# Kernel optimization log

Measured on AMD Instinct MI355X. Metric: run time of the kernel, lower is better.

## Reference

```python
import jax, jax.numpy as jnp
import numpy as np

# Architecture constants (match init_kwargs)
STEPS, BATCH = 256, 128
IN_SIZE, H1, H2, OUT = 512, 1536, 1536, 512
DELAY = 1


def setup_inputs() -> dict:
    key = jax.random.key(0)
    ks = jax.random.split(key, 5)
    def init_w(k, shape):
        fan_in = shape[0]
        return (jax.random.normal(k, shape, jnp.float32) / np.sqrt(fan_in).astype(np.float32))
    return {
        "inputs": jax.random.normal(ks[0], (STEPS, BATCH, IN_SIZE), jnp.float32),
        # hidden1 RNNC: in = sizes['#input'] + sizes['hidden1'] (self-recurrent conn)
        "W1": init_w(ks[1], (IN_SIZE + H1, H1)),
        "b1": jnp.zeros((H1,), jnp.float32),
        # hidden2 RNNC: in = sizes['hidden1'] + sizes['hidden2']
        "W2": init_w(ks[2], (H1 + H2, H2)),
        "b2": jnp.zeros((H2,), jnp.float32),
        # '##output' PlaceholderWt: linear readout from hidden2
        "Wo": init_w(ks[3], (H2, OUT)),
        "bo": jnp.zeros((OUT,), jnp.float32),
    }


def reference(inputs, W1, b1, W2, b2, Wo, bo):
    # Stepped multi-layer RNN with delay=1 spike buffers.
    # Within a step, layers update in order, so a layer reading spikes_all[-1]
    # of an EARLIER layer sees the current step's spike, while self/backward
    # connections see the previous step's spike (carried through the scan).
    B = inputs.shape[1]

    def step(carry, x_t):
        s_h1_prev, s_h2_prev = carry
        s_in = x_t                                               # Placeholder '#input'
        # hidden1: prevs = ['#input' (current), 'hidden1' (prev step)]
        s_h1 = jnp.tanh(jnp.concatenate([s_in, s_h1_prev], -1) @ W1 + b1)
        # hidden2: prevs = ['hidden1' (current), 'hidden2' (prev step)]
        s_h2 = jnp.tanh(jnp.concatenate([s_h1, s_h2_prev], -1) @ W2 + b2)
        # '##output' PlaceholderWt: linear readout of current hidden2 spike
        out = s_h2 @ Wo + bo
        return (s_h1, s_h2), out

    init = (jnp.zeros((B, H1), inputs.dtype), jnp.zeros((B, H2), inputs.dtype))
    _, outs = jax.lax.scan(step, init, inputs)                   # [steps, B, OUT]
    # spikes_all includes `delay` initial zero spikes from reset_state
    zeros = jnp.zeros((DELAY, B, OUT), inputs.dtype)
    return jnp.concatenate([zeros, outs], axis=0)                # [delay+steps, B, OUT]
```

## Files before the change

kernel.cpp:

```cpp
#include <hip/hip_runtime.h>
#include <math.h>

#define STEPS 256
#define BATCH 128
#define HALF_M 64
#define INSZ  512
#define H1SZ  1536
#define H2SZ  1536
#define NOUT  512
#define K1    2048
#define K2    3072
#define NC1   48
#define NC2   48
#define NC3   16
#define NBLK  224

typedef short bf16x8 __attribute__((ext_vector_type(8)));
typedef float f32x4  __attribute__((ext_vector_type(4)));
typedef unsigned short u16;

__device__ __forceinline__ f32x4 mfma16(bf16x8 a, bf16x8 b, f32x4 c) {
  return __builtin_amdgcn_mfma_f32_16x16x32_bf16(a, b, c, 0, 0, 0);
}

__device__ __forceinline__ u16 f2bf(float f) {
  unsigned u = __builtin_bit_cast(unsigned, f);
  u += 0x7fffu + ((u >> 16) & 1u);
  return (u16)(u >> 16);
}

__device__ __forceinline__ bf16x8 cvt8(const float* p) {
  f32x4 lo = *(const f32x4*)p;
  f32x4 hi = *(const f32x4*)(p + 4);
  union { unsigned u[4]; bf16x8 v; } r;
  asm("v_cvt_pk_bf16_f32 %0, %1, %2" : "=v"(r.u[0]) : "v"(lo[0]), "v"(lo[1]));
  asm("v_cvt_pk_bf16_f32 %0, %1, %2" : "=v"(r.u[1]) : "v"(lo[2]), "v"(lo[3]));
  asm("v_cvt_pk_bf16_f32 %0, %1, %2" : "=v"(r.u[2]) : "v"(hi[0]), "v"(hi[1]));
  asm("v_cvt_pk_bf16_f32 %0, %1, %2" : "=v"(r.u[3]) : "v"(hi[2]), "v"(hi[3]));
  return r.v;
}

#define LOAD_SC_OFS(dst, ptr, ofs) \
  asm volatile("global_load_dwordx4 %0, %1, off offset:%2 sc0 sc1" \
               : "=v"(dst) : "v"(ptr), "i"(ofs) : "memory")
#define STORE_SC(ptr, val) \
  asm volatile("global_store_dwordx4 %0, %1, off sc0 sc1" :: "v"(ptr), "v"(val) : "memory")
#define WAITV(n) asm volatile("s_waitcnt vmcnt(" #n ")" ::: "memory")
#define PIN4(v) asm volatile("" : "+v"(v))

__device__ __forceinline__ void set_flag(int* p, int v) {
  __hip_atomic_store(p, v, __ATOMIC_RELAXED, __HIP_MEMORY_SCOPE_SYSTEM);
}

__device__ __forceinline__ void wave_wait(const int* p, int tgt, bool active) {
  while (true) {
    int v = __hip_atomic_load(p, __ATOMIC_RELAXED, __HIP_MEMORY_SCOPE_SYSTEM);
    if (!__any(active && (v < tgt))) break;
    __builtin_amdgcn_s_sleep(1);
  }
}

__device__ __forceinline__ void kloop12(const u16* base, const bf16x8 (*Br)[2],
                                        f32x4 (*acc)[2], int r16) {
  const u16* rp[4];
#pragma unroll
  for (int mf = 0; mf < 4; ++mf) rp[mf] = base + (size_t)(mf * 16 + r16) * 1536;
  bf16x8 A[8][4];
  WAITV(0);
#pragma unroll
  for (int d = 0; d < 8; ++d)
#pragma unroll
    for (int mf = 0; mf < 4; ++mf)
      LOAD_SC_OFS(A[d][mf], rp[mf], d * 64);
#pragma unroll
  for (int ks = 0; ks < 12; ++ks) {
    const int rem = (11 - ks) < 7 ? (11 - ks) : 7;
    if (rem == 7)      WAITV(28);
    else if (rem == 6) WAITV(24);
    else if (rem == 5) WAITV(20);
    else if (rem == 4) WAITV(16);
    else if (rem == 3) WAITV(12);
    else if (rem == 2) WAITV(8);
    else if (rem == 1) WAITV(4);
    else               WAITV(0);
    __builtin_amdgcn_sched_barrier(0);
#pragma unroll
    for (int mf = 0; mf < 4; ++mf) {
      acc[mf][0] = mfma16(A[ks & 7][mf], Br[ks][0], acc[mf][0]);
      acc[mf][1] = mfma16(A[ks & 7][mf], Br[ks][1], acc[mf][1]);
    }
    if (ks < 4) {
#pragma unroll
      for (int mf = 0; mf < 4; ++mf)
        LOAD_SC_OFS(A[ks & 7][mf], rp[mf], (ks + 8) * 64);
    }
  }
}

__device__ __forceinline__ void kloop_x4(const float* xb, const bf16x8 (*Br)[2],
                                         f32x4 (*acc)[2], int r16) {
#pragma unroll
  for (int ks = 0; ks < 4; ++ks)
#pragma unroll
    for (int mf = 0; mf < 4; ++mf) {
      bf16x8 a = cvt8(xb + (size_t)(mf * 16 + r16) * INSZ + ks * 32);
      acc[mf][0] = mfma16(a, Br[ks][0], acc[mf][0]);
      acc[mf][1] = mfma16(a, Br[ks][1], acc[mf][1]);
    }
}

__device__ __forceinline__ void store_red(float (*red)[64][36], int kw, int kg, int r16,
                                          const f32x4 (*acc)[2]) {
#pragma unroll
  for (int mf = 0; mf < 4; ++mf)
#pragma unroll
    for (int nf = 0; nf < 2; ++nf)
#pragma unroll
      for (int r = 0; r < 4; ++r)
        red[kw][mf * 16 + kg * 4 + r][nf * 16 + r16] = acc[mf][nf][r];
}

__device__ __forceinline__ void epi_tanh(const float (*red)[64][36], f32x4 bv0, f32x4 bv1,
                                         u16* dstbase, int n0, int tid) {
  const int row = tid >> 2, c0 = (tid & 3) * 8;
  f32x4 s0 = bv0, s1 = bv1;
#pragma unroll
  for (int w = 0; w < 4; ++w) {
    s0 += *(const f32x4*)&red[w][row][c0];
    s1 += *(const f32x4*)&red[w][row][c0 + 4];
  }
  float t[8];
#pragma unroll
  for (int j = 0; j < 4; ++j) t[j] = tanhf(s0[j]);
#pragma unroll
  for (int j = 0; j < 4; ++j) t[4 + j] = tanhf(s1[j]);
  union { unsigned u[4]; bf16x8 v; } pk;
  asm("v_cvt_pk_bf16_f32 %0, %1, %2" : "=v"(pk.u[0]) : "v"(t[0]), "v"(t[1]));
  asm("v_cvt_pk_bf16_f32 %0, %1, %2" : "=v"(pk.u[1]) : "v"(t[2]), "v"(t[3]));
  asm("v_cvt_pk_bf16_f32 %0, %1, %2" : "=v"(pk.u[2]) : "v"(t[4]), "v"(t[5]));
  asm("v_cvt_pk_bf16_f32 %0, %1, %2" : "=v"(pk.u[3]) : "v"(t[6]), "v"(t[7]));
  u16* dst = dstbase + (size_t)row * 1536 + n0 + c0;
  STORE_SC(dst, pk.v);
}

__global__ __launch_bounds__(256)
__attribute__((amdgpu_waves_per_eu(1, 1)))
void rnn_main(
    const float* __restrict__ x,
    const u16* __restrict__ W1T, const u16* __restrict__ W2T, const u16* __restrict__ WoT,
    const float* __restrict__ b1, const float* __restrict__ b2, const float* __restrict__ bo,
    u16* __restrict__ h1ring, u16* __restrict__ h2ring,
    float* __restrict__ out, int* __restrict__ bar)
{
  __shared__ float red[4][64][36];
  const int tid = threadIdx.x;
  const int kw = tid >> 6, lane = tid & 63;
  const int r16 = lane & 15, kg = lane >> 4;
  const int bid = blockIdx.x;

  int grp, half, col;
  if (bid < 2 * NC1)              { grp = 0; half = bid / NC1;         col = bid % NC1; }
  else if (bid < 2 * (NC1 + NC2)) { grp = 1; half = (bid - 96) / NC2;  col = (bid - 96) % NC2; }
  else                            { grp = 2; half = (bid - 192) / NC3; col = (bid - 192) % NC3; }
  const int n0 = col * 32;
  int* f1 = bar + (half * NC1) * 16;
  int* f2 = bar + (96 + half * NC2) * 16;
  int* f3 = bar + (192 + half * NC3) * 16;

  u16* h1base = h1ring + (size_t)half * 4 * HALF_M * H1SZ;
  u16* h2base = h2ring + (size_t)half * 4 * HALF_M * H2SZ;

  const int* wpA = f1; int dA = 0; bool aA = false;
  const int* wpB = f1; int dB = 0; bool aB = false;
  if (grp == 0) {
    if (lane < 12)                      { wpA = f1 + (kw * 12 + lane) * 16; dA = 0;  aA = true; }
    else if (kw == 0 && lane >= 16)     { wpA = f2 + (lane - 16) * 16;      dA = -3; aA = true; }
  } else if (grp == 1) {
    if (lane < 12) {
      wpA = f2 + (kw * 12 + lane) * 16; dA = 0; aA = true;
      wpB = f1 + (kw * 12 + lane) * 16; dB = 1; aB = true;
    } else if (kw == 0 && lane >= 32 && lane < 48) {
      wpA = f3 + (lane - 32) * 16; dA = -3; aA = true;
    }
  } else {
    if (lane < 12)                      { wpA = f2 + (kw * 12 + lane) * 16; dA = 1;  aA = true; }
  }

  if (grp == 0) {
    bf16x8 BrX[4][2], Brh[12][2];
#pragma unroll
    for (int ks = 0; ks < 4; ++ks)
#pragma unroll
      for (int nf = 0; nf < 2; ++nf)
        BrX[ks][nf] = *(const bf16x8*)(W1T + (size_t)(n0 + nf * 16 + r16) * K1
                                       + kw * 128 + ks * 32 + kg * 8);
#pragma unroll
    for (int ks = 0; ks < 12; ++ks)
#pragma unroll
      for (int nf = 0; nf < 2; ++nf)
        Brh[ks][nf] = *(const bf16x8*)(W1T + (size_t)(n0 + nf * 16 + r16) * K1
                                       + 512 + kw * 384 + ks * 32 + kg * 8);
#pragma unroll
    for (int ks = 0; ks < 4; ++ks) { PIN4(BrX[ks][0]); PIN4(BrX[ks][1]); }
#pragma unroll
    for (int ks = 0; ks < 12; ++ks) { PIN4(Brh[ks][0]); PIN4(Brh[ks][1]); }
    const f32x4 bv0 = *(const f32x4*)(b1 + n0 + (tid & 3) * 8);
    const f32x4 bv1 = *(const f32x4*)(b1 + n0 + (tid & 3) * 8 + 4);

    for (int k = 0; k < STEPS; ++k) {
      f32x4 acc[4][2] = {};
      const float* xb = x + ((size_t)k * BATCH + half * HALF_M) * INSZ + kw * 128 + kg * 8;
      kloop_x4(xb, BrX, acc, r16);
      wave_wait(wpA, k + dA, aA);
      kloop12(h1base + (size_t)((k + 3) & 3) * HALF_M * H1SZ + kw * 384 + kg * 8,
              Brh, acc, r16);
      store_red(red, kw, kg, r16, acc);
      __syncthreads();
      epi_tanh(red, bv0, bv1, h1base + (size_t)(k & 3) * HALF_M * H1SZ, n0, tid);
      WAITV(0);
      __syncthreads();
      if (tid == 0) set_flag(&f1[col * 16], k + 1);
    }
  } else if (grp == 1) {
    bf16x8 Bh2[12][2], Bh1[12][2];
#pragma unroll
    for (int ks = 0; ks < 12; ++ks)
#pragma unroll
      for (int nf = 0; nf < 2; ++nf) {
        Bh2[ks][nf] = *(const bf16x8*)(W2T + (size_t)(n0 + nf * 16 + r16) * K2
                                       + 1536 + kw * 384 + ks * 32 + kg * 8);
        Bh1[ks][nf] = *(const bf16x8*)(W2T + (size_t)(n0 + nf * 16 + r16) * K2
                                       + kw * 384 + ks * 32 + kg * 8);
      }
#pragma unroll
    for (int ks = 0; ks < 12; ++ks) { PIN4(Bh2[ks][0]); PIN4(Bh2[ks][1]);
                                      PIN4(Bh1[ks][0]); PIN4(Bh1[ks][1]); }
    const f32x4 bv0 = *(const f32x4*)(b2 + n0 + (tid & 3) * 8);
    const f32x4 bv1 = *(const f32x4*)(b2 + n0 + (tid & 3) * 8 + 4);

    for (int j = 0; j < STEPS; ++j) {
      f32x4 acc[4][2] = {};
      wave_wait(wpA, j + dA, aA);
      kloop12(h2base + (size_t)((j + 3) & 3) * HALF_M * H2SZ + kw * 384 + kg * 8,
              Bh2, acc, r16);
      wave_wait(wpB, j + dB, aB);
      kloop12(h1base + (size_t)(j & 3) * HALF_M * H1SZ + kw * 384 + kg * 8,
              Bh1, acc, r16);
      store_red(red, kw, kg, r16, acc);
      __syncthreads();
      epi_tanh(red, bv0, bv1, h2base + (size_t)(j & 3) * HALF_M * H2SZ, n0, tid);
      WAITV(0);
      __syncthreads();
      if (tid == 0) set_flag(&f2[col * 16], j + 1);
    }
  } else {
    bf16x8 Br[12][2];
#pragma unroll
    for (int ks = 0; ks < 12; ++ks)
#pragma unroll
      for (int nf = 0; nf < 2; ++nf)
        Br[ks][nf] = *(const bf16x8*)(WoT + (size_t)(n0 + nf * 16 + r16) * H2SZ
                                      + kw * 384 + ks * 32 + kg * 8);
#pragma unroll
    for (int ks = 0; ks < 12; ++ks) { PIN4(Br[ks][0]); PIN4(Br[ks][1]); }
    const f32x4 bv0 = *(const f32x4*)(bo + n0 + (tid & 3) * 8);
    const f32x4 bv1 = *(const f32x4*)(bo + n0 + (tid & 3) * 8 + 4);

    for (int j = 0; j < STEPS; ++j) {
      f32x4 acc[4][2] = {};
      wave_wait(wpA, j + dA, aA);
      kloop12(h2base + (size_t)(j & 3) * HALF_M * H2SZ + kw * 384 + kg * 8,
              Br, acc, r16);
      store_red(red, kw, kg, r16, acc);
      __syncthreads();
      {
        const int row = tid >> 2, c0 = (tid & 3) * 8;
        f32x4 s0 = bv0, s1 = bv1;
#pragma unroll
        for (int w = 0; w < 4; ++w) {
          s0 += *(const f32x4*)&red[w][row][c0];
          s1 += *(const f32x4*)&red[w][row][c0 + 4];
        }
        float* dst = out + ((size_t)(j + 1) * BATCH + half * HALF_M + row) * NOUT + n0 + c0;
        *(f32x4*)dst = s0;
        *(f32x4*)(dst + 4) = s1;
      }
      __syncthreads();
      if (tid == 0) set_flag(&f3[col * 16], j + 1);
    }
  }
}

__global__ void transpose_cvt(const float* __restrict__ src, u16* __restrict__ dst, int K, int N) {
  __shared__ u16 tile[32][33];
  int kb = blockIdx.x * 32, nb = blockIdx.y * 32;
  int tx = threadIdx.x & 31, ty = threadIdx.x >> 5;
  for (int i = ty; i < 32; i += 8)
    tile[i][tx] = f2bf(src[(size_t)(kb + i) * N + nb + tx]);
  __syncthreads();
  for (int i = ty; i < 32; i += 8)
    dst[(size_t)(nb + i) * K + kb + tx] = tile[tx][i];
}

extern "C" void kernel_launch(void* const* d_in, const int* in_sizes, int n_in,
                              void* d_out, int out_size, void* d_ws, size_t ws_size,
                              hipStream_t stream) {
  const float* x  = (const float*)d_in[0];
  const float* W1 = (const float*)d_in[1];
  const float* b1 = (const float*)d_in[2];
  const float* W2 = (const float*)d_in[3];
  const float* b2 = (const float*)d_in[4];
  const float* Wo = (const float*)d_in[5];
  const float* bo = (const float*)d_in[6];
  float* out = (float*)d_out;
  char*  ws  = (char*)d_ws;

  u16* W1T    = (u16*)(ws);
  u16* W2T    = (u16*)(ws + 6291456);
  u16* WoT    = (u16*)(ws + 15728640);
  u16* h1ring = (u16*)(ws + 17301504);
  u16* h2ring = (u16*)(ws + 18874368);
  int* bar    = (int*)(ws + 20447232);

  hipMemsetAsync(ws + 17301504, 0, 1572864 * 2 + 14336, stream);
  hipMemsetAsync(d_out, 0, (size_t)BATCH * NOUT * sizeof(float), stream);

  transpose_cvt<<<dim3(K1 / 32, H1SZ / 32), 256, 0, stream>>>(W1, W1T, K1, H1SZ);
  transpose_cvt<<<dim3(K2 / 32, H1SZ / 32), 256, 0, stream>>>(W2, W2T, K2, H1SZ);
  transpose_cvt<<<dim3(H2SZ / 32, NOUT / 32), 256, 0, stream>>>(Wo, WoT, H2SZ, NOUT);

  rnn_main<<<NBLK, 256, 0, stream>>>(x, W1T, W2T, WoT, b1, b2, bo, h1ring, h2ring, out, bar);
}
```

Measured before the change: 3.544 ms.

## Deepen hidden-state rings to 8, keep weights in AGPRs, issue all loads upfront

Grows the h1/h2 ring buffers from 4 to 8 slots and relaxes the producer back-pressure waits from -3 to -6 steps, so upstream layers can run further ahead of consumers. Recurrent weight fragments are moved into accumulation registers and fed to inline-asm MFMA with an AGPR B operand, which frees VGPRs so all 12 k-slices of activations can be loaded at once instead of through an 8-deep rolling window. Adds manual s_nop hazard fences and doubles workspace use; the inline asm bypasses compiler hazard tracking, so the fences must be sufficient.

After: 3.407 ms. -3.9%, faster.

```diff
diff --git a/kernel.cpp b/kernel.cpp
--- a/kernel.cpp
+++ b/kernel.cpp
@@ -14,6 +14,7 @@
 #define NC2   48
 #define NC3   16
 #define NBLK  224
+#define RING  8
 
 typedef short bf16x8 __attribute__((ext_vector_type(8)));
 typedef float f32x4  __attribute__((ext_vector_type(4)));
@@ -46,7 +47,11 @@
 #define STORE_SC(ptr, val) \
   asm volatile("global_store_dwordx4 %0, %1, off sc0 sc1" :: "v"(ptr), "v"(val) : "memory")
 #define WAITV(n) asm volatile("s_waitcnt vmcnt(" #n ")" ::: "memory")
-#define PIN4(v) asm volatile("" : "+v"(v))
+#define PIN4(v)  asm volatile("" : "+v"(v))
+#define PINA(v)  asm volatile("" : "+a"(v))
+#define MFMA_AB(acc, va, ab) \
+  asm volatile("v_mfma_f32_16x16x32_bf16 %0, %1, %2, %0" : "+v"(acc) : "v"(va), "a"(ab))
+#define MFMA_FENCE() asm volatile("s_nop 7\n\ts_nop 7\n\ts_nop 7")
 
 __device__ __forceinline__ void set_flag(int* p, int v) {
   __hip_atomic_store(p, v, __ATOMIC_RELAXED, __HIP_MEMORY_SCOPE_SYSTEM);
@@ -60,45 +65,45 @@
   }
 }
 
-__device__ __forceinline__ void kloop12(const u16* base, const bf16x8 (*Br)[2],
-                                        f32x4 (*acc)[2], int r16) {
+__device__ __forceinline__ void kloop12a(const u16* base, const bf16x8 (&Ba)[12][2],
+                                         f32x4 (&acc)[4][2], int r16) {
   const u16* rp[4];
 #pragma unroll
   for (int mf = 0; mf < 4; ++mf) rp[mf] = base + (size_t)(mf * 16 + r16) * 1536;
-  bf16x8 A[8][4];
+  bf16x8 A[12][4];
   WAITV(0);
 #pragma unroll
-  for (int d = 0; d < 8; ++d)
+  for (int d = 0; d < 12; ++d)
 #pragma unroll
     for (int mf = 0; mf < 4; ++mf)
       LOAD_SC_OFS(A[d][mf], rp[mf], d * 64);
 #pragma unroll
   for (int ks = 0; ks < 12; ++ks) {
-    const int rem = (11 - ks) < 7 ? (11 - ks) : 7;
-    if (rem == 7)      WAITV(28);
-    else if (rem == 6) WAITV(24);
-    else if (rem == 5) WAITV(20);
-    else if (rem == 4) WAITV(16);
-    else if (rem == 3) WAITV(12);
-    else if (rem == 2) WAITV(8);
-    else if (rem == 1) WAITV(4);
-    else               WAITV(0);
+    const int rem = 11 - ks;
+    if (rem == 11)      WAITV(44);
+    else if (rem == 10) WAITV(40);
+    else if (rem == 9)  WAITV(36);
+    else if (rem == 8)  WAITV(32);
+    else if (rem == 7)  WAITV(28);
+    else if (rem == 6)  WAITV(24);
+    else if (rem == 5)  WAITV(20);
+    else if (rem == 4)  WAITV(16);
+    else if (rem == 3)  WAITV(12);
+    else if (rem == 2)  WAITV(8);
+    else if (rem == 1)  WAITV(4);
+    else                WAITV(0);
     __builtin_amdgcn_sched_barrier(0);
 #pragma unroll
     for (int mf = 0; mf < 4; ++mf) {
-      acc[mf][0] = mfma16(A[ks & 7][mf], Br[ks][0], acc[mf][0]);
-      acc[mf][1] = mfma16(A[ks & 7][mf], Br[ks][1], acc[mf][1]);
-    }
-    if (ks < 4) {
-#pragma unroll
-      for (int mf = 0; mf < 4; ++mf)
-        LOAD_SC_OFS(A[ks & 7][mf], rp[mf], (ks + 8) * 64);
-    }
-  }
-}
-
-__device__ __forceinline__ void kloop_x4(const float* xb, const bf16x8 (*Br)[2],
-                                         f32x4 (*acc)[2], int r16) {
+      MFMA_AB(acc[mf][0], A[ks][mf], Ba[ks][0]);
+      MFMA_AB(acc[mf][1], A[ks][mf], Ba[ks][1]);
+    }
+  }
+  MFMA_FENCE();
+}
+
+__device__ __forceinline__ void kloop_x4(const float* xb, const bf16x8 (&Br)[4][2],
+                                         f32x4 (&acc)[4][2], int r16) {
 #pragma unroll
   for (int ks = 0; ks < 4; ++ks)
 #pragma unroll
@@ -110,7 +115,7 @@
 }
 
 __device__ __forceinline__ void store_red(float (*red)[64][36], int kw, int kg, int r16,
-                                          const f32x4 (*acc)[2]) {
+                                          const f32x4 (&acc)[4][2]) {
 #pragma unroll
   for (int mf = 0; mf < 4; ++mf)
 #pragma unroll
@@ -167,23 +172,23 @@
   int* f2 = bar + (96 + half * NC2) * 16;
   int* f3 = bar + (192 + half * NC3) * 16;
 
-  u16* h1base = h1ring + (size_t)half * 4 * HALF_M * H1SZ;
-  u16* h2base = h2ring + (size_t)half * 4 * HALF_M * H2SZ;
+  u16* h1base = h1ring + (size_t)half * RING * HALF_M * H1SZ;
+  u16* h2base = h2ring + (size_t)half * RING * HALF_M * H2SZ;
 
   const int* wpA = f1; int dA = 0; bool aA = false;
   const int* wpB = f1; int dB = 0; bool aB = false;
   if (grp == 0) {
-    if (lane < 12)                      { wpA = f1 + (kw * 12 + lane) * 16; dA = 0;  aA = true; }
-    else if (kw == 0 && lane >= 16)     { wpA = f2 + (lane - 16) * 16;      dA = -3; aA = true; }
+    if (lane < 12)                  { wpA = f1 + (kw * 12 + lane) * 16; dA = 0;  aA = true; }
+    else if (kw == 0 && lane >= 16) { wpA = f2 + (lane - 16) * 16;      dA = -6; aA = true; }
   } else if (grp == 1) {
     if (lane < 12) {
       wpA = f2 + (kw * 12 + lane) * 16; dA = 0; aA = true;
       wpB = f1 + (kw * 12 + lane) * 16; dB = 1; aB = true;
     } else if (kw == 0 && lane >= 32 && lane < 48) {
-      wpA = f3 + (lane - 32) * 16; dA = -3; aA = true;
+      wpA = f3 + (lane - 32) * 16; dA = -6; aA = true;
     }
   } else {
-    if (lane < 12)                      { wpA = f2 + (kw * 12 + lane) * 16; dA = 1;  aA = true; }
+    if (lane < 12)                  { wpA = f2 + (kw * 12 + lane) * 16; dA = 1;  aA = true; }
   }
 
   if (grp == 0) {
@@ -203,7 +208,8 @@
 #pragma unroll
     for (int ks = 0; ks < 4; ++ks) { PIN4(BrX[ks][0]); PIN4(BrX[ks][1]); }
 #pragma unroll
-    for (int ks = 0; ks < 12; ++ks) { PIN4(Brh[ks][0]); PIN4(Brh[ks][1]); }
+    for (int ks = 0; ks < 12; ++ks) { PINA(Brh[ks][0]); PINA(Brh[ks][1]); }
+    asm volatile("s_nop 7\n\ts_nop 7");
     const f32x4 bv0 = *(const f32x4*)(b1 + n0 + (tid & 3) * 8);
     const f32x4 bv1 = *(const f32x4*)(b1 + n0 + (tid & 3) * 8 + 4);
 
@@ -212,11 +218,11 @@
       const float* xb = x + ((size_t)k * BATCH + half * HALF_M) * INSZ + kw * 128 + kg * 8;
       kloop_x4(xb, BrX, acc, r16);
       wave_wait(wpA, k + dA, aA);
-      kloop12(h1base + (size_t)((k + 3) & 3) * HALF_M * H1SZ + kw * 384 + kg * 8,
-              Brh, acc, r16);
+      kloop12a(h1base + (size_t)((k + RING - 1) & (RING - 1)) * HALF_M * H1SZ
+               + kw * 384 + kg * 8, Brh, acc, r16);
       store_red(red, kw, kg, r16, acc);
       __syncthreads();
-      epi_tanh(red, bv0, bv1, h1base + (size_t)(k & 3) * HALF_M * H1SZ, n0, tid);
+      epi_tanh(red, bv0, bv1, h1base + (size_t)(k & (RING - 1)) * HALF_M * H1SZ, n0, tid);
       WAITV(0);
       __syncthreads();
       if (tid == 0) set_flag(&f1[col * 16], k + 1);
@@ -233,22 +239,23 @@
                                        + kw * 384 + ks * 32 + kg * 8);
       }
 #pragma unroll
-    for (int ks = 0; ks < 12; ++ks) { PIN4(Bh2[ks][0]); PIN4(Bh2[ks][1]);
-                                      PIN4(Bh1[ks][0]); PIN4(Bh1[ks][1]); }
+    for (int ks = 0; ks < 12; ++ks) { PINA(Bh2[ks][0]); PINA(Bh2[ks][1]);
+                                      PINA(Bh1[ks][0]); PINA(Bh1[ks][1]); }
+    asm volatile("s_nop 7\n\ts_nop 7");
     const f32x4 bv0 = *(const f32x4*)(b2 + n0 + (tid & 3) * 8);
     const f32x4 bv1 = *(const f32x4*)(b2 + n0 + (tid & 3) * 8 + 4);
 
     for (int j = 0; j < STEPS; ++j) {
       f32x4 acc[4][2] = {};
       wave_wait(wpA, j + dA, aA);
-      kloop12(h2base + (size_t)((j + 3) & 3) * HALF_M * H2SZ + kw * 384 + kg * 8,
-              Bh2, acc, r16);
+      kloop12a(h2base + (size_t)((j + RING - 1) & (RING - 1)) * HALF_M * H2SZ
+               + kw * 384 + kg * 8, Bh2, acc, r16);
       wave_wait(wpB, j + dB, aB);
-      kloop12(h1base + (size_t)(j & 3) * HALF_M * H1SZ + kw * 384 + kg * 8,
-              Bh1, acc, r16);
+      kloop12a(h1base + (size_t)(j & (RING - 1)) * HALF_M * H1SZ
+               + kw * 384 + kg * 8, Bh1, acc, r16);
       store_red(red, kw, kg, r16, acc);
       __syncthreads();
-      epi_tanh(red, bv0, bv1, h2base + (size_t)(j & 3) * HALF_M * H2SZ, n0, tid);
+      epi_tanh(red, bv0, bv1, h2base + (size_t)(j & (RING - 1)) * HALF_M * H2SZ, n0, tid);
       WAITV(0);
       __syncthreads();
       if (tid == 0) set_flag(&f2[col * 16], j + 1);
@@ -262,15 +269,16 @@
         Br[ks][nf] = *(const bf16x8*)(WoT + (size_t)(n0 + nf * 16 + r16) * H2SZ
                                       + kw * 384 + ks * 32 + kg * 8);
 #pragma unroll
-    for (int ks = 0; ks < 12; ++ks) { PIN4(Br[ks][0]); PIN4(Br[ks][1]); }
+    for (int ks = 0; ks < 12; ++ks) { PINA(Br[ks][0]); PINA(Br[ks][1]); }
+    asm volatile("s_nop 7\n\ts_nop 7");
     const f32x4 bv0 = *(const f32x4*)(bo + n0 + (tid & 3) * 8);
     const f32x4 bv1 = *(const f32x4*)(bo + n0 + (tid & 3) * 8 + 4);
 
     for (int j = 0; j < STEPS; ++j) {
       f32x4 acc[4][2] = {};
       wave_wait(wpA, j + dA, aA);
-      kloop12(h2base + (size_t)(j & 3) * HALF_M * H2SZ + kw * 384 + kg * 8,
-              Br, acc, r16);
+      kloop12a(h2base + (size_t)(j & (RING - 1)) * HALF_M * H2SZ
+               + kw * 384 + kg * 8, Br, acc, r16);
       store_red(red, kw, kg, r16, acc);
       __syncthreads();
       {
@@ -319,10 +327,10 @@
   u16* W2T    = (u16*)(ws + 6291456);
   u16* WoT    = (u16*)(ws + 15728640);
   u16* h1ring = (u16*)(ws + 17301504);
-  u16* h2ring = (u16*)(ws + 18874368);
-  int* bar    = (int*)(ws + 20447232);
-
-  hipMemsetAsync(ws + 17301504, 0, 1572864 * 2 + 14336, stream);
+  u16* h2ring = (u16*)(ws + 20447232);
+  int* bar    = (int*)(ws + 23592960);
+
+  hipMemsetAsync(ws + 17301504, 0, 3145728 * 2 + 14336, stream);
   hipMemsetAsync(d_out, 0, (size_t)BATCH * NOUT * sizeof(float), stream);
 
   transpose_cvt<<<dim3(K1 / 32, H1SZ / 32), 256, 0, stream>>>(W1, W1T, K1, H1SZ);
```
